# Performance work log

Measured on AMD Instinct MI355X. Metric: run time of the kernel, lower is better.

Reference implementation:

```python
import jax, jax.numpy as jnp
import numpy as np
from jax import lax

K = 9
CENTER = K // 2
EXTEND = 1.0
EPS = 1e-5
GROUPS = 16  # out_ch // 4


def conv2d(x, w, b, stride, padding):
    y = lax.conv_general_dilated(x, w, window_strides=stride, padding=padding,
                                 dimension_numbers=('NCHW', 'OIHW', 'NCHW'))
    return y + b[None, :, None, None]


def setup_inputs() -> dict:
    key = jax.random.key(0)
    ks = jax.random.split(key, 9)
    B, C, Wd, Hd, OUT = 8, 64, 128, 128, 64
    f = jax.random.normal(ks[0], (B, C, Wd, Hd), jnp.float32)
    w_off = jax.random.normal(ks[1], (2 * K, C, 3, 3), jnp.float32) * 0.05
    b_off = jax.random.normal(ks[2], (2 * K,), jnp.float32) * 0.05
    bn_gamma = 1.0 + 0.1 * jax.random.normal(ks[3], (2 * K,), jnp.float32)
    bn_beta = 0.1 * jax.random.normal(ks[4], (2 * K,), jnp.float32)
    w_dsc = jax.random.normal(ks[5], (OUT, C, K, 1), jnp.float32) * 0.05
    b_dsc = jax.random.normal(ks[6], (OUT,), jnp.float32) * 0.05
    gn_gamma = 1.0 + 0.1 * jax.random.normal(ks[7], (OUT,), jnp.float32)
    gn_beta = 0.1 * jax.random.normal(ks[8], (OUT,), jnp.float32)
    return {'f': f, 'w_off': w_off, 'b_off': b_off, 'bn_gamma': bn_gamma,
            'bn_beta': bn_beta, 'w_dsc': w_dsc, 'b_dsc': b_dsc,
            'gn_gamma': gn_gamma, 'gn_beta': gn_beta}


def _forward(f, w_off, b_off, bn_gamma, bn_beta, w_dsc, b_dsc, gn_gamma, gn_beta):
    B, C, Wd, Hd = f.shape  # module names: width=shape[2], height=shape[3]
    dt = f.dtype

    # offset branch: conv3x3 -> BatchNorm (training mode, batch stats) -> tanh
    off = conv2d(f, w_off, b_off, (1, 1), 'SAME')
    mu = off.mean(axis=(0, 2, 3), keepdims=True)
    var = off.var(axis=(0, 2, 3), keepdims=True)
    off = (off - mu) / jnp.sqrt(var + EPS)
    off = off * bn_gamma[None, :, None, None] + bn_beta[None, :, None, None]
    off = jnp.tanh(off)

    y_off = off[:, :K]  # [B,K,Wd,Hd]; x_off (off[:, K:]) unused for morph=0

    # cumulative offset scan from the center point (morph=0).
    # NOTE: endpoints 0 and K-1 keep detached raw offsets (torch detach().clone()).
    raw0 = lax.stop_gradient(y_off)
    offn = [None] * K
    offn[CENTER] = jnp.zeros_like(y_off[:, 0])
    for i in range(1, CENTER):
        offn[CENTER + i] = offn[CENTER + i - 1] + y_off[:, CENTER + i]
        offn[CENTER - i] = offn[CENTER - i + 1] + y_off[:, CENTER - i]
    offn[0] = raw0[:, 0]
    offn[K - 1] = raw0[:, K - 1]
    offn = jnp.stack(offn, axis=1)  # [B,K,Wd,Hd]

    # coordinate grids: y indexes the width axis, x the height axis
    y_new = jnp.arange(Wd, dtype=dt)[None, None, :, None] + offn * EXTEND  # [B,K,Wd,Hd]
    x_new = ((jnp.arange(K, dtype=dt) - CENTER)[None, :, None, None]
             + jnp.arange(Hd, dtype=dt)[None, None, None, :])  # [1,K,1,Hd]
    x_new = jnp.broadcast_to(x_new, (B, K, Wd, Hd))

    # layout [B, K*Wd, Hd] via (B,K,Wd,Hd) -> (B,Wd,K,Hd)
    y_s = jnp.transpose(y_new, (0, 2, 1, 3)).reshape(B, K * Wd * Hd)
    x_s = jnp.transpose(x_new, (0, 2, 1, 3)).reshape(B, K * Wd * Hd)

    # bilinear interpolation (clamped corner indices, unclamped y/x in weights)
    y0 = jnp.floor(y_s).astype(jnp.int32)
    x0 = jnp.floor(x_s).astype(jnp.int32)
    y0c = jnp.clip(y0, 0, Wd - 1)
    y1c = jnp.clip(y0 + 1, 0, Wd - 1)
    x0c = jnp.clip(x0, 0, Hd - 1)
    x1c = jnp.clip(x0 + 1, 0, Hd - 1)

    feat = jnp.transpose(f, (0, 2, 3, 1)).reshape(B, Wd * Hd, C)

    def gather(yi, xi):
        idx = (yi * Hd + xi)[:, :, None]  # [B,N,1]
        return jnp.take_along_axis(feat, idx, axis=1)  # [B,N,C]

    va0 = gather(y0c, x0c)
    vc0 = gather(y0c, x1c)
    va1 = gather(y1c, x0c)
    vc1 = gather(y1c, x1c)

    y0f, y1f = y0c.astype(dt), y1c.astype(dt)
    x0f, x1f = x0c.astype(dt), x1c.astype(dt)
    wa = ((y1f - y_s) * (x1f - x_s))[:, :, None]
    wb = ((y1f - y_s) * (x_s - x0f))[:, :, None]
    wc = ((y_s - y0f) * (x1f - x_s))[:, :, None]
    wd = ((y_s - y0f) * (x_s - x0f))[:, :, None]

    out = va0 * wa + vc0 * wb + va1 * wc + vc1 * wd  # [B,N,C]
    deformed = jnp.transpose(out.reshape(B, K * Wd, Hd, C), (0, 3, 1, 2))  # [B,C,K*Wd,Hd]

    # strided conv over the K snake points -> [B,OUT,Wd,Hd]
    x = conv2d(deformed, w_dsc, b_dsc, (K, 1), 'VALID')

    # GroupNorm + ReLU
    OUT = x.shape[1]
    xg = x.reshape(B, GROUPS, -1)
    gmu = xg.mean(axis=-1, keepdims=True)
    gvar = xg.var(axis=-1, keepdims=True)
    xg = (xg - gmu) / jnp.sqrt(gvar + EPS)
    x = xg.reshape(x.shape) * gn_gamma[None, :, None, None] + gn_beta[None, :, None, None]
    return jax.nn.relu(x)


def reference(f, w_off, b_off, bn_gamma, bn_beta, w_dsc, b_dsc, gn_gamma, gn_beta):
    return _forward(f, w_off, b_off, bn_gamma, bn_beta, w_dsc, b_dsc, gn_gamma, gn_beta)
```

## Files before the change

### kernel.cpp

```cpp
#include <hip/hip_runtime.h>

#define B_   8
#define C_   64
#define W_   128
#define H_   128
#define K_   9
#define OUT_ 64
#define NPIX (B_*W_*H_)
#define EPS_ 1e-5f

typedef __attribute__((ext_vector_type(8))) short bf16x8;
typedef __attribute__((ext_vector_type(4))) float f32x4;

#define FEATBF_OFF  0
#define XPRE_OFF    4194304
#define OFFPRE_OFF  12582912
#define OFFH_OFF    13762560
#define WT_OFF      16121856
#define WP_OFF      16140288
#define BNSTATS_OFF 16145472
#define BNAB_OFF    16145490
#define GSTATS_OFF  16145508
#define GNFIN_OFF   16145764
#define STATS_BYTES ((18+18+256+256)*sizeof(float))

__device__ __forceinline__ unsigned pack2bf(float a, float b) {
    union { float f; unsigned u; } ua, ub;
    ua.f = a; ub.f = b;
    unsigned x = ua.u, y = ub.u;
    x += 0x7fffu + ((x >> 16) & 1u);
    y += 0x7fffu + ((y >> 16) & 1u);
    return (x >> 16) | (y & 0xffff0000u);
}
__device__ __forceinline__ float bflo(unsigned u) {
    union { unsigned u; float f; } v; v.u = u << 16; return v.f;
}
__device__ __forceinline__ float bfhi(unsigned u) {
    union { unsigned u; float f; } v; v.u = u & 0xffff0000u; return v.f;
}

__global__ __launch_bounds__(256) void k_nhwc(const float* __restrict__ f,
                                              unsigned short* __restrict__ featbf) {
    __shared__ float tile[64][65];
    int bid = blockIdx.x;
    int ht = bid & 1;
    int w  = (bid >> 1) & 127;
    int b  = bid >> 8;
    int t  = threadIdx.x;
    int lh = t & 63;
    int c0 = (t >> 6) * 16;
    const float* fp = f + (((b*64)*128 + w)*128) + ht*64 + lh;
#pragma unroll
    for (int i = 0; i < 16; i++) {
        int c = c0 + i;
        tile[c][lh] = fp[c*16384];
    }
    __syncthreads();
    int lc = t & 63;
    int h0 = (t >> 6) * 16;
    unsigned short* obf = featbf + ((size_t)((b*128 + w)*128) + ht*64)*64 + lc;
#pragma unroll
    for (int i = 0; i < 16; i++) {
        int hr = h0 + i;
        union { float f; unsigned u; } v; v.f = tile[lc][hr];
        unsigned x = v.u + 0x7fffu + ((v.u >> 16) & 1u);
        obf[(size_t)hr*64] = (unsigned short)(x >> 16);
    }
}

__global__ void k_wt(const float* __restrict__ w_dsc, unsigned short* __restrict__ wTbf) {
    int i = blockIdx.x*256 + threadIdx.x;
    if (i >= 9*64*64) return;
    int c = i & 63;
    int o = (i >> 6) & 63;
    int k = i >> 12;
    union { float f; unsigned u; } v;
    v.f = w_dsc[(o*64 + c)*9 + k];
    unsigned x = v.u + 0x7fffu + ((v.u >> 16) & 1u);
    wTbf[i] = (unsigned short)(x >> 16);
}

__global__ void k_wp(const float* __restrict__ w_off, float* __restrict__ wP) {
    int i = blockIdx.x*256 + threadIdx.x;
    if (i >= 64*81) return;
    int c    = i / 81;
    int rem  = i % 81;
    int dw   = rem / 27;
    int rem2 = rem % 27;
    int ck   = rem2 / 3;
    int dh   = rem2 % 3;
    wP[i] = w_off[ck*576 + c*9 + dw*3 + dh];
}

__global__ __launch_bounds__(128) void k_conv_off(const float* __restrict__ f,
                                                  const float* __restrict__ wP,
                                                  float* __restrict__ off_half) {
    int t   = threadIdx.x;
    int bid = blockIdx.x;
    int b   = bid & 7;
    int w   = (bid >> 3) & 127;
    int ch  = bid >> 10;
    int h   = t;

    float em = (h == 0)   ? 0.f : 1.f;
    float ep = (h == 127) ? 0.f : 1.f;
    int   om = h + ((h == 0)   ? 0 : -1);
    int   op = h + ((h == 127) ? 0 : 1);

    const float* fb = f + (size_t)b*1048576 + (size_t)(ch*32)*16384 + (size_t)w*128;
    const float* wb = wP + ch*32*81;

    float acc[9];
#pragma unroll
    for (int ck = 0; ck < 9; ck++) acc[ck] = 0.f;

#pragma unroll 4
    for (int c = 0; c < 32; c++) {
        const float* p  = fb + c*16384;
        const float* wc = wb + c*81;
#pragma unroll
        for (int dw = -1; dw <= 1; dw++) {
            int wy = w + dw;
            if ((unsigned)wy < 128u) {
                const float* q = p + dw*128;
                float v0 = q[om] * em;
                float v1 = q[h];
                float v2 = q[op] * ep;
                const float* ww = wc + (dw+1)*27;
#pragma unroll
                for (int ck = 0; ck < 9; ck++)
                    acc[ck] += v0*ww[ck*3] + v1*ww[ck*3+1] + v2*ww[ck*3+2];
            }
        }
    }

    float* dst = off_half + (size_t)ch*1179648;
    int pixoff = (w << 7) + h;
#pragma unroll
    for (int ck = 0; ck < 9; ck++)
        dst[((b*9 + ck) << 14) + pixoff] = acc[ck];
}

__global__ __launch_bounds__(256) void k_bn_stats(const float* __restrict__ off_half,
                                                  float* __restrict__ off_pre,
                                                  float* __restrict__ bnstats) {
    __shared__ float wred[4][2];
    int bid = blockIdx.x;
    int b  = bid / 36;
    int rem = bid % 36;
    int ck = rem / 4;
    int wq = rem % 4;
    int t  = threadIdx.x;
    int base4 = (((b*9+ck) << 14) + wq*4096) >> 2;

    const float4* h0 = (const float4*)off_half;
    const float4* h1 = (const float4*)(off_half + 1179648);
    float4* op = (float4*)off_pre;

    float s = 0.f, q = 0.f;
#pragma unroll
    for (int i = 0; i < 4; i++) {
        int idx = base4 + t + i*256;
        float4 a = h0[idx], bb = h1[idx];
        float4 v;
        v.x = a.x + bb.x; v.y = a.y + bb.y; v.z = a.z + bb.z; v.w = a.w + bb.w;
        op[idx] = v;
        s += v.x + v.y + v.z + v.w;
        q += v.x*v.x + v.y*v.y + v.z*v.z + v.w*v.w;
    }
    for (int off = 32; off; off >>= 1) {
        s += __shfl_down(s, off);
        q += __shfl_down(q, off);
    }
    if ((t & 63) == 0) { wred[t >> 6][0] = s; wred[t >> 6][1] = q; }
    __syncthreads();
    if (t == 0) atomicAdd(&bnstats[ck*2],   wred[0][0]+wred[1][0]+wred[2][0]+wred[3][0]);
    if (t == 1) atomicAdd(&bnstats[ck*2+1], wred[0][1]+wred[1][1]+wred[2][1]+wred[3][1]);
}

__global__ void k_bn_fin(const float* __restrict__ bnstats,
                         const float* __restrict__ bn_gamma,
                         const float* __restrict__ bn_beta,
                         float* __restrict__ bnAB) {
    int t = threadIdx.x;
    if (t < 9) {
        float n    = (float)NPIX;
        float mean = bnstats[t*2] / n;
        float var  = bnstats[t*2+1] / n - mean*mean;
        float A    = bn_gamma[t] / sqrtf(var + EPS_);
        bnAB[t*2]   = A;
        bnAB[t*2+1] = bn_beta[t] - mean * A;
    }
}

__global__ __launch_bounds__(256) void k_sample_dsc(const unsigned short* __restrict__ featbf,
                                                    const float* __restrict__ off_pre,
                                                    const float* __restrict__ bnAB,
                                                    const unsigned short* __restrict__ wTbf,
                                                    const float* __restrict__ b_dsc,
                                                    float* __restrict__ xpre,
                                                    float* __restrict__ gstats) {
    __shared__ __align__(16) unsigned char lds_samp[128*128];
    __shared__ __align__(16) unsigned char lds_wk[64*128];
    __shared__ float ynew[9][128];
    __shared__ float red[16][2];

    int t = threadIdx.x;
    int b = blockIdx.x & 7, w = blockIdx.x >> 3;

    if (t < 128) {
        int h = t;
        float y[9];
#pragma unroll
        for (int ck = 0; ck < 9; ck++) {
            float v = off_pre[((b*9+ck) << 14) + (w << 7) + h];
            y[ck] = tanhf(bnAB[ck*2]*v + bnAB[ck*2+1]);
        }
        float ofn[9];
        ofn[4] = 0.f;
        ofn[5] = y[5]; ofn[6] = y[5]+y[6]; ofn[7] = y[5]+y[6]+y[7];
        ofn[3] = y[3]; ofn[2] = y[3]+y[2]; ofn[1] = y[3]+y[2]+y[1];
        ofn[0] = y[0]; ofn[8] = y[8];
#pragma unroll
        for (int k = 0; k < 9; k++) ynew[k][h] = (float)w + ofn[k];
    }
    if (t < 16) { red[t][0] = 0.f; red[t][1] = 0.f; }

    f32x4 acc[2][4];
#pragma unroll
    for (int mi = 0; mi < 2; mi++)
#pragma unroll
        for (int ni = 0; ni < 4; ni++) {
            acc[mi][ni][0] = 0.f; acc[mi][ni][1] = 0.f;
            acc[mi][ni][2] = 0.f; acc[mi][ni][3] = 0.f;
        }

    int lane = t & 63, wv = t >> 6;
    int m0 = wv * 32;
    int lm = lane & 15, lk = lane >> 4;
    int hs = t >> 1;
    int cq = (t & 1) * 4;

    __syncthreads();

    for (int k = 0; k < 9; k++) {
        if (k) __syncthreads();

        {
            const uint4* src = (const uint4*)(wTbf + (k << 12));
#pragma unroll
            for (int i = 0; i < 2; i++) {
                int ci = t + i*256;
                uint4 v = src[ci];
                int o  = ci >> 3;
                int cb = (ci & 7) << 4;
                *(uint4*)(lds_wk + o*128 + (cb ^ ((o & 7) << 4))) = v;
            }
        }

        {
            int x0 = k - 4 + hs;
            unsigned char* dst = lds_samp + hs*128;
            int bcol0 = (t & 1) * 64;
            if ((unsigned)x0 < 127u) {
                float ys = ynew[k][hs];
                int y0  = (int)floorf(ys);
                int y0c = min(max(y0, 0), 127), y1c = min(max(y0+1, 0), 127);
                float wa = (float)y1c - ys;
                float wc = ys - (float)y0c;
                const unsigned short* pb = featbf + ((size_t)b << 20);
                const uint4* p0 = (const uint4*)(pb + (y0c*128 + x0)*64) + cq;
                const uint4* p1 = (const uint4*)(pb + (y1c*128 + x0)*64) + cq;
#pragma unroll
                for (int ci = 0; ci < 4; ci++) {
                    uint4 a = p0[ci], c = p1[ci];
                    uint4 u;
                    u.x = pack2bf(bflo(a.x)*wa + bflo(c.x)*wc, bfhi(a.x)*wa + bfhi(c.x)*wc);
                    u.y = pack2bf(bflo(a.y)*wa + bflo(c.y)*wc, bfhi(a.y)*wa + bfhi(c.y)*wc);
                    u.z = pack2bf(bflo(a.z)*wa + bflo(c.z)*wc, bfhi(a.z)*wa + bfhi(c.z)*wc);
                    u.w = pack2bf(bflo(a.w)*wa + bflo(c.w)*wc, bfhi(a.w)*wa + bfhi(c.w)*wc);
                    *(uint4*)(dst + ((bcol0 + ci*16) ^ ((hs & 7) << 4))) = u;
                }
            } else {
                uint4 z = make_uint4(0,0,0,0);
#pragma unroll
                for (int ci = 0; ci < 4; ci++)
                    *(uint4*)(dst + ((bcol0 + ci*16) ^ ((hs & 7) << 4))) = z;
            }
        }
        __syncthreads();

#pragma unroll
        for (int ks = 0; ks < 2; ks++) {
            bf16x8 af[2], bfr[4];
#pragma unroll
            for (int mi = 0; mi < 2; mi++) {
                int h = m0 + mi*16 + lm;
                af[mi] = *(const bf16x8*)(lds_samp + h*128 + ((ks*64 + lk*16) ^ ((h & 7) << 4)));
            }
#pragma unroll
            for (int ni = 0; ni < 4; ni++) {
                int o = ni*16 + lm;
                bfr[ni] = *(const bf16x8*)(lds_wk + o*128 + ((ks*64 + lk*16) ^ ((o & 7) << 4)));
            }
#pragma unroll
            for (int mi = 0; mi < 2; mi++)
#pragma unroll
                for (int ni = 0; ni < 4; ni++)
                    acc[mi][ni] = __builtin_amdgcn_mfma_f32_16x16x32_bf16(af[mi], bfr[ni], acc[mi][ni], 0, 0, 0);
        }
    }

#pragma unroll
    for (int ni = 0; ni < 4; ni++) {
        int o = ni*16 + lm;
        float bias = b_dsc[o];
        float s1 = 0.f, s2 = 0.f;
#pragma unroll
        for (int mi = 0; mi < 2; mi++) {
            float4 r;
            r.x = acc[mi][ni][0] + bias;
            r.y = acc[mi][ni][1] + bias;
            r.z = acc[mi][ni][2] + bias;
            r.w = acc[mi][ni][3] + bias;
            s1 += r.x + r.y + r.z + r.w;
            s2 += r.x*r.x + r.y*r.y + r.z*r.z + r.w*r.w;
            int h = m0 + mi*16 + lk*4;
            *(float4*)(xpre + (((b*64 + o) << 14) + (w << 7) + h)) = r;
        }
        s1 += __shfl_xor(s1, 1);  s1 += __shfl_xor(s1, 2);
        s1 += __shfl_xor(s1, 16); s1 += __shfl_xor(s1, 32);
        s2 += __shfl_xor(s2, 1);  s2 += __shfl_xor(s2, 2);
        s2 += __shfl_xor(s2, 16); s2 += __shfl_xor(s2, 32);
        if (lk == 0 && (lm & 3) == 0) {
            atomicAdd(&red[ni*4 + (lm >> 2)][0], s1);
            atomicAdd(&red[ni*4 + (lm >> 2)][1], s2);
        }
    }
    __syncthreads();
    if (t < 16) {
        atomicAdd(&gstats[(b*16 + t)*2],   red[t][0]);
        atomicAdd(&gstats[(b*16 + t)*2+1], red[t][1]);
    }
}

__global__ void k_gn_fin(const float* __restrict__ gstats, float* __restrict__ gnfin) {
    int t = threadIdx.x;
    if (t < 128) {
        float n    = 65536.f;
        float mean = gstats[t*2] / n;
        float var  = gstats[t*2+1] / n - mean*mean;
        gnfin[t*2]   = mean;
        gnfin[t*2+1] = 1.0f / sqrtf(var + EPS_);
    }
}

__global__ __launch_bounds__(256) void k_gn_apply(const float* __restrict__ xpre,
                                                  const float* __restrict__ gnfin,
                                                  const float* __restrict__ gn_gamma,
                                                  const float* __restrict__ gn_beta,
                                                  float* __restrict__ out) {
    int i4  = blockIdx.x*256 + threadIdx.x;
    int idx = i4 * 4;
    int o = (idx >> 14) & 63;
    int b = idx >> 20;
    int g = o >> 2;
    float mean = gnfin[(b*16+g)*2];
    float istd = gnfin[(b*16+g)*2+1];
    float ga = gn_gamma[o] * istd;
    float be = gn_beta[o] - mean * ga;
    float4 v = *(const float4*)(xpre + idx);
    v.x = fmaxf(v.x*ga + be, 0.f);
    v.y = fmaxf(v.y*ga + be, 0.f);
    v.z = fmaxf(v.z*ga + be, 0.f);
    v.w = fmaxf(v.w*ga + be, 0.f);
    *(float4*)(out + idx) = v;
}

extern "C" void kernel_launch(void* const* d_in, const int* in_sizes, int n_in,
                              void* d_out, int out_size, void* d_ws, size_t ws_size,
                              hipStream_t stream) {
    const float* f        = (const float*)d_in[0];
    const float* w_off    = (const float*)d_in[1];
    const float* bn_gamma = (const float*)d_in[3];
    const float* bn_beta  = (const float*)d_in[4];
    const float* w_dsc    = (const float*)d_in[5];
    const float* b_dsc    = (const float*)d_in[6];
    const float* gn_gamma = (const float*)d_in[7];
    const float* gn_beta  = (const float*)d_in[8];

    float* ws      = (float*)d_ws;
    unsigned short* featbf = (unsigned short*)(ws + FEATBF_OFF);
    float* xpre    = ws + XPRE_OFF;
    float* off_pre = ws + OFFPRE_OFF;
    float* off_half= ws + OFFH_OFF;
    unsigned short* wTbf = (unsigned short*)(ws + WT_OFF);
    float* wP      = ws + WP_OFF;
    float* bnstats = ws + BNSTATS_OFF;
    float* bnAB    = ws + BNAB_OFF;
    float* gstats  = ws + GSTATS_OFF;
    float* gnfin   = ws + GNFIN_OFF;

    hipMemsetAsync(bnstats, 0, STATS_BYTES, stream);

    k_nhwc<<<2048, 256, 0, stream>>>(f, featbf);
    k_wt<<<144, 256, 0, stream>>>(w_dsc, wTbf);
    k_wp<<<21, 256, 0, stream>>>(w_off, wP);
    k_conv_off<<<2048, 128, 0, stream>>>(f, wP, off_half);
    k_bn_stats<<<288, 256, 0, stream>>>(off_half, off_pre, bnstats);
    k_bn_fin<<<1, 32, 0, stream>>>(bnstats, bn_gamma, bn_beta, bnAB);
    k_sample_dsc<<<1024, 256, 0, stream>>>(featbf, off_pre, bnAB, wTbf, b_dsc, xpre, gstats);
    k_gn_fin<<<1, 128, 0, stream>>>(gstats, gnfin);
    k_gn_apply<<<8192, 256, 0, stream>>>(xpre, gnfin, gn_gamma, gn_beta, (float*)d_out);
}
```

Before: 124.1 us.

## Split offset conv into four channel quarters, shuffle halo, store pre-GN output as bf16

The offset conv now splits input channels four ways instead of two, doubling the grid, and gets left/right neighbours through warp shuffles instead of extra global loads. The BN stats kernel sums four partial buffers. The pre-GroupNorm intermediate is stored in bf16 instead of fp32, halving its write and read traffic in the sample and GN-apply kernels. This adds rounding error before normalization and extra partial-sum traffic for the offset branch.

```diff
diff --git a/kernel.cpp b/kernel.cpp
--- a/kernel.cpp
+++ b/kernel.cpp
@@ -14,14 +14,14 @@
 
 #define FEATBF_OFF  0
 #define XPRE_OFF    4194304
-#define OFFPRE_OFF  12582912
-#define OFFH_OFF    13762560
-#define WT_OFF      16121856
-#define WP_OFF      16140288
-#define BNSTATS_OFF 16145472
-#define BNAB_OFF    16145490
-#define GSTATS_OFF  16145508
-#define GNFIN_OFF   16145764
+#define OFFPRE_OFF  8388608
+#define OFFH_OFF    9568256
+#define WT_OFF      14286848
+#define WP_OFF      14305280
+#define BNSTATS_OFF 14310464
+#define BNAB_OFF    14310482
+#define GSTATS_OFF  14310500
+#define GNFIN_OFF   14310756
 #define STATS_BYTES ((18+18+256+256)*sizeof(float))
 
 __device__ __forceinline__ unsigned pack2bf(float a, float b) {
@@ -99,23 +99,21 @@
     int bid = blockIdx.x;
     int b   = bid & 7;
     int w   = (bid >> 3) & 127;
-    int ch  = bid >> 10;
+    int cq  = bid >> 10;
     int h   = t;
 
     float em = (h == 0)   ? 0.f : 1.f;
     float ep = (h == 127) ? 0.f : 1.f;
-    int   om = h + ((h == 0)   ? 0 : -1);
-    int   op = h + ((h == 127) ? 0 : 1);
-
-    const float* fb = f + (size_t)b*1048576 + (size_t)(ch*32)*16384 + (size_t)w*128;
-    const float* wb = wP + ch*32*81;
+
+    const float* fb = f + (size_t)b*1048576 + (size_t)(cq*16)*16384 + (size_t)w*128;
+    const float* wb = wP + cq*16*81;
 
     float acc[9];
 #pragma unroll
     for (int ck = 0; ck < 9; ck++) acc[ck] = 0.f;
 
 #pragma unroll 4
-    for (int c = 0; c < 32; c++) {
+    for (int c = 0; c < 16; c++) {
         const float* p  = fb + c*16384;
         const float* wc = wb + c*81;
 #pragma unroll
@@ -123,9 +121,12 @@
             int wy = w + dw;
             if ((unsigned)wy < 128u) {
                 const float* q = p + dw*128;
-                float v0 = q[om] * em;
                 float v1 = q[h];
-                float v2 = q[op] * ep;
+                float v0 = __shfl_up(v1, 1);
+                float v2 = __shfl_down(v1, 1);
+                if (t == 64) v0 = q[63];
+                if (t == 63) v2 = q[64];
+                v0 *= em; v2 *= ep;
                 const float* ww = wc + (dw+1)*27;
 #pragma unroll
                 for (int ck = 0; ck < 9; ck++)
@@ -134,7 +135,7 @@
         }
     }
 
-    float* dst = off_half + (size_t)ch*1179648;
+    float* dst = off_half + (size_t)cq*1179648;
     int pixoff = (w << 7) + h;
 #pragma unroll
     for (int ck = 0; ck < 9; ck++)
@@ -155,15 +156,20 @@
 
     const float4* h0 = (const float4*)off_half;
     const float4* h1 = (const float4*)(off_half + 1179648);
+    const float4* h2 = (const float4*)(off_half + 2359296);
+    const float4* h3 = (const float4*)(off_half + 3538944);
     float4* op = (float4*)off_pre;
 
     float s = 0.f, q = 0.f;
 #pragma unroll
     for (int i = 0; i < 4; i++) {
         int idx = base4 + t + i*256;
-        float4 a = h0[idx], bb = h1[idx];
+        float4 a = h0[idx], bb = h1[idx], cc = h2[idx], dd = h3[idx];
         float4 v;
-        v.x = a.x + bb.x; v.y = a.y + bb.y; v.z = a.z + bb.z; v.w = a.w + bb.w;
+        v.x = (a.x + bb.x) + (cc.x + dd.x);
+        v.y = (a.y + bb.y) + (cc.y + dd.y);
+        v.z = (a.z + bb.z) + (cc.z + dd.z);
+        v.w = (a.w + bb.w) + (cc.w + dd.w);
         op[idx] = v;
         s += v.x + v.y + v.z + v.w;
         q += v.x*v.x + v.y*v.y + v.z*v.z + v.w*v.w;
@@ -198,7 +204,7 @@
                                                     const float* __restrict__ bnAB,
                                                     const unsigned short* __restrict__ wTbf,
                                                     const float* __restrict__ b_dsc,
-                                                    float* __restrict__ xpre,
+                                                    unsigned short* __restrict__ xprebf,
                                                     float* __restrict__ gstats) {
     __shared__ __align__(16) unsigned char lds_samp[128*128];
     __shared__ __align__(16) unsigned char lds_wk[64*128];
@@ -326,7 +332,10 @@
             s1 += r.x + r.y + r.z + r.w;
             s2 += r.x*r.x + r.y*r.y + r.z*r.z + r.w*r.w;
             int h = m0 + mi*16 + lk*4;
-            *(float4*)(xpre + (((b*64 + o) << 14) + (w << 7) + h)) = r;
+            uint2 u2;
+            u2.x = pack2bf(r.x, r.y);
+            u2.y = pack2bf(r.z, r.w);
+            *(uint2*)(xprebf + (((b*64 + o) << 14) + (w << 7) + h)) = u2;
         }
         s1 += __shfl_xor(s1, 1);  s1 += __shfl_xor(s1, 2);
         s1 += __shfl_xor(s1, 16); s1 += __shfl_xor(s1, 32);
@@ -355,13 +364,13 @@
     }
 }
 
-__global__ __launch_bounds__(256) void k_gn_apply(const float* __restrict__ xpre,
+__global__ __launch_bounds__(256) void k_gn_apply(const unsigned short* __restrict__ xprebf,
                                                   const float* __restrict__ gnfin,
                                                   const float* __restrict__ gn_gamma,
                                                   const float* __restrict__ gn_beta,
                                                   float* __restrict__ out) {
-    int i4  = blockIdx.x*256 + threadIdx.x;
-    int idx = i4 * 4;
+    int i8  = blockIdx.x*256 + threadIdx.x;
+    int idx = i8 * 8;
     int o = (idx >> 14) & 63;
     int b = idx >> 20;
     int g = o >> 2;
@@ -369,12 +378,18 @@
     float istd = gnfin[(b*16+g)*2+1];
     float ga = gn_gamma[o] * istd;
     float be = gn_beta[o] - mean * ga;
-    float4 v = *(const float4*)(xpre + idx);
-    v.x = fmaxf(v.x*ga + be, 0.f);
-    v.y = fmaxf(v.y*ga + be, 0.f);
-    v.z = fmaxf(v.z*ga + be, 0.f);
-    v.w = fmaxf(v.w*ga + be, 0.f);
-    *(float4*)(out + idx) = v;
+    uint4 v = *(const uint4*)(xprebf + idx);
+    float4 r0, r1;
+    r0.x = fmaxf(bflo(v.x)*ga + be, 0.f);
+    r0.y = fmaxf(bfhi(v.x)*ga + be, 0.f);
+    r0.z = fmaxf(bflo(v.y)*ga + be, 0.f);
+    r0.w = fmaxf(bfhi(v.y)*ga + be, 0.f);
+    r1.x = fmaxf(bflo(v.z)*ga + be, 0.f);
+    r1.y = fmaxf(bfhi(v.z)*ga + be, 0.f);
+    r1.z = fmaxf(bflo(v.w)*ga + be, 0.f);
+    r1.w = fmaxf(bfhi(v.w)*ga + be, 0.f);
+    *(float4*)(out + idx)     = r0;
+    *(float4*)(out + idx + 4) = r1;
 }
 
 extern "C" void kernel_launch(void* const* d_in, const int* in_sizes, int n_in,
@@ -391,7 +406,7 @@
 
     float* ws      = (float*)d_ws;
     unsigned short* featbf = (unsigned short*)(ws + FEATBF_OFF);
-    float* xpre    = ws + XPRE_OFF;
+    unsigned short* xprebf = (unsigned short*)(ws + XPRE_OFF);
     float* off_pre = ws + OFFPRE_OFF;
     float* off_half= ws + OFFH_OFF;
     unsigned short* wTbf = (unsigned short*)(ws + WT_OFF);
@@ -406,10 +421,10 @@
     k_nhwc<<<2048, 256, 0, stream>>>(f, featbf);
     k_wt<<<144, 256, 0, stream>>>(w_dsc, wTbf);
     k_wp<<<21, 256, 0, stream>>>(w_off, wP);
-    k_conv_off<<<2048, 128, 0, stream>>>(f, wP, off_half);
+    k_conv_off<<<4096, 128, 0, stream>>>(f, wP, off_half);
     k_bn_stats<<<288, 256, 0, stream>>>(off_half, off_pre, bnstats);
     k_bn_fin<<<1, 32, 0, stream>>>(bnstats, bn_gamma, bn_beta, bnAB);
-    k_sample_dsc<<<1024, 256, 0, stream>>>(featbf, off_pre, bnAB, wTbf, b_dsc, xpre, gstats);
+    k_sample_dsc<<<1024, 256, 0, stream>>>(featbf, off_pre, bnAB, wTbf, b_dsc, xprebf, gstats);
     k_gn_fin<<<1, 128, 0, stream>>>(gstats, gnfin);
-    k_gn_apply<<<8192, 256, 0, stream>>>(xpre, gnfin, gn_gamma, gn_beta, (float*)d_out);
-}
+    k_gn_apply<<<4096, 256, 0, stream>>>(xprebf, gnfin, gn_gamma, gn_beta, (float*)d_out);
+}
```

Measured after the change: 123.0 us. Within noise of the previous version (-0.9%).
